# Kernel optimization log

Hardware: AMD Instinct MI355X
Metric: run time of the kernel (lower is better)

The kernel has to match this reference:

```python
import jax, jax.numpy as jnp
import numpy as np

N, E, C, H, L = 50000, 800000, 128, 2, 2  # nodes, edges, hidden_dim, heads, layers
NEG_SLOPE = 0.2
BN_EPS = 1e-5


def setup_inputs() -> dict:
    key = jax.random.key(0)
    ks = jax.random.split(key, 7)
    s = 1.0 / np.sqrt(C).astype(np.float32)
    x = jax.random.normal(ks[0], (N, C), jnp.float32)
    edge_index = jax.random.randint(ks[1], (2, E), 0, N, dtype=jnp.int64)
    W = jax.random.normal(ks[2], (L, C, H * C), jnp.float32) * s      # per-layer lin weight
    att_src = jax.random.normal(ks[3], (L, H, C), jnp.float32) * s    # a_src
    att_dst = jax.random.normal(ks[4], (L, H, C), jnp.float32) * s    # a_dst
    bias = jnp.zeros((L, C), jnp.float32)                              # GATConv bias
    gamma = jnp.ones((L, C), jnp.float32)                              # BatchNorm weight
    beta = jnp.zeros((L, C), jnp.float32)                              # BatchNorm bias
    return dict(x=x, edge_index=edge_index, W=W, att_src=att_src,
                att_dst=att_dst, bias=bias, gamma=gamma, beta=beta)


def _gat_layer(x, src, dst, W, a_src, a_dst, b):
    # Linear projection, split heads: [N, H, C]
    h = (x @ W).reshape(N, H, C)
    # Per-node attention logits, [N, H]
    al_s = jnp.sum(h * a_src[None], axis=-1)
    al_d = jnp.sum(h * a_dst[None], axis=-1)
    # Per-edge raw scores [E', H] (E' includes self loops)
    e = jax.nn.leaky_relu(al_s[src] + al_d[dst], NEG_SLOPE)
    # Segment softmax over incoming edges of each destination node
    m = jax.ops.segment_max(e, dst, num_segments=N)
    ex = jnp.exp(e - m[dst])
    denom = jax.ops.segment_sum(ex, dst, num_segments=N)
    alpha = ex / denom[dst]
    # Weighted scatter-add aggregation: [N, H, C]
    out = jax.ops.segment_sum(alpha[:, :, None] * h[src], dst, num_segments=N)
    # concat=False -> mean over heads, then bias
    return out.mean(axis=1) + b


def _batchnorm(x, g, bt):
    mu = x.mean(axis=0)
    var = jnp.mean((x - mu) ** 2, axis=0)  # biased var (torch BN training math)
    return g * (x - mu) * jax.lax.rsqrt(var + BN_EPS) + bt


def reference(x, edge_index, W, att_src, att_dst, bias, gamma, beta):
    loops = jnp.arange(N, dtype=edge_index.dtype)
    src = jnp.concatenate([edge_index[0], loops])  # add_self_loops=True
    dst = jnp.concatenate([edge_index[1], loops])
    for l in range(L):
        res = x
        x = _gat_layer(x, src, dst, W[l], att_src[l], att_dst[l], bias[l])
        x = _batchnorm(x, gamma[l], beta[l])
        x = jax.nn.elu(x)
        x = x + res  # use_residual, residual_proj = Identity
    return x
```

## Files before the change

### kernel.cpp

```cpp
#include <hip/hip_runtime.h>
#include <hip/hip_bf16.h>

#define N_NODES 50000
#define N_EDGES 800000
#define TOT_E (N_EDGES + N_NODES)
#define PS 256
#define NP ((N_NODES + PS - 1) / PS)
#define BCAP 6000
#define NBK 256
#define BCHUNK ((TOT_E + NBK - 1) / NBK)

typedef unsigned short us8 __attribute__((ext_vector_type(8)));
typedef short s16x8 __attribute__((ext_vector_type(8)));
typedef float f32x4 __attribute__((ext_vector_type(4)));

static __device__ __forceinline__ float lrelu(float v) { return v > 0.0f ? v : 0.2f * v; }

static __device__ __forceinline__ unsigned short f2bf(float f) {
    unsigned int u = __float_as_uint(f);
    unsigned int r = (u + 0x7FFF + ((u >> 16) & 1)) >> 16;
    return (unsigned short)r;
}
static __device__ __forceinline__ float bf2f(unsigned short u) {
    return __uint_as_float(((unsigned int)u) << 16);
}

__global__ __launch_bounds__(256) void bucket_kernel(const int* __restrict__ ei,
                                                     int* __restrict__ gcur,
                                                     unsigned int* __restrict__ buckets) {
    __shared__ int hist[NP];
    __shared__ int runb[NP];
    __shared__ unsigned int pk[BCHUNK + 7];
    int tid = threadIdx.x;
    for (int t = tid; t < NP; t += 256) hist[t] = 0;
    __syncthreads();
    int lo = blockIdx.x * BCHUNK;
    int hi = lo + BCHUNK < TOT_E ? lo + BCHUNK : TOT_E;
    for (int base = lo; base < lo + BCHUNK; base += 256) {
        int i = base + tid;
        if (i < hi) {
            int s, d;
            if (i < N_EDGES) { s = ei[i]; d = ei[N_EDGES + i]; }
            else { s = d = i - N_EDGES; }
            pk[i - lo] = ((unsigned)d << 16) | (unsigned)s;
            atomicAdd(&hist[d >> 8], 1);
        }
    }
    __syncthreads();
    for (int t = tid; t < NP; t += 256) runb[t] = atomicAdd(&gcur[t], hist[t]);
    __syncthreads();
    for (int base = lo; base < lo + BCHUNK; base += 256) {
        int i = base + tid;
        if (i < hi) {
            unsigned v = pk[i - lo];
            int p = v >> 24;
            int slot = atomicAdd(&runb[p], 1);
            if (slot < BCAP) buckets[(size_t)p * BCAP + slot] = v;
        }
    }
}

__global__ __launch_bounds__(256) void csr_kernel(const int* __restrict__ gcur,
                                                  const unsigned int* __restrict__ buckets,
                                                  int* __restrict__ pbeg, int* __restrict__ pend,
                                                  unsigned short* __restrict__ srcs) {
    __shared__ unsigned int epk[BCAP];
    __shared__ unsigned short sl[BCAP];
    __shared__ int deg[256], ps[256], cur[256];
    int p = blockIdx.x, tid = threadIdx.x;
    int len = gcur[p];
    if (len > BCAP) len = BCAP;
    deg[tid] = 0;
    __syncthreads();
    for (int j = tid; j < len; j += 256) {
        unsigned v = buckets[(size_t)p * BCAP + j];
        epk[j] = v;
        atomicAdd(&deg[(v >> 16) & 255], 1);
    }
    __syncthreads();
    int v0 = deg[tid];
    ps[tid] = v0;
    __syncthreads();
#pragma unroll
    for (int o = 1; o < 256; o <<= 1) {
        int u = (tid >= o) ? ps[tid - o] : 0;
        __syncthreads();
        ps[tid] += u;
        __syncthreads();
    }
    int lbeg = ps[tid] - v0;
    cur[tid] = lbeg;
    int n = p * PS + tid;
    if (n < N_NODES) {
        pbeg[n] = p * BCAP + lbeg;
        pend[n] = p * BCAP + lbeg + v0;
    }
    __syncthreads();
    for (int j = tid; j < len; j += 256) {
        unsigned v = epk[j];
        int slot = atomicAdd(&cur[(v >> 16) & 255], 1);
        sl[slot] = (unsigned short)(v & 0xFFFF);
    }
    __syncthreads();
    for (int j = tid; j < len; j += 256) srcs[(size_t)p * BCAP + j] = sl[j];
}

__global__ __launch_bounds__(256) void wa_kernel(const float* __restrict__ W, const float* __restrict__ as_,
                                                 const float* __restrict__ ad_, float* __restrict__ was,
                                                 float* __restrict__ wad) {
    int l = blockIdx.x;
    int t = threadIdx.x;
    int head = t >> 7, k = t & 127;
    const float* wr = W + (size_t)l * 32768 + (size_t)k * 256 + head * 128;
    const float* ar = as_ + l * 256 + head * 128;
    const float* dr = ad_ + l * 256 + head * 128;
    float s = 0.f, d = 0.f;
    for (int c = 0; c < 128; ++c) {
        float wv = wr[c];
        s += wv * ar[c];
        d += wv * dr[c];
    }
    was[l * 256 + t] = s;
    wad[l * 256 + t] = d;
}

__global__ __launch_bounds__(256) void mt_kernel(const float* __restrict__ W, unsigned short* __restrict__ Mt) {
    int idx = blockIdx.x * 256 + threadIdx.x;
    int l = idx >> 15, c = (idx >> 8) & 127, kc = idx & 255;
    int head = kc >> 7, k = kc & 127;
    Mt[idx] = f2bf(0.5f * W[(size_t)l * 32768 + (size_t)k * 256 + head * 128 + c]);
}

__global__ __launch_bounds__(256) void convert_kernel(const float* __restrict__ x, unsigned short* __restrict__ xb,
                                                      const float* __restrict__ was, const float* __restrict__ wad,
                                                      float2* __restrict__ als, float2* __restrict__ ald) {
    int idx = blockIdx.x * 256 + threadIdx.x;
    int n = idx >> 5;
    int c4 = (idx & 31) * 4;
    float4 v = *(const float4*)(x + (size_t)n * 128 + c4);
    ushort4 o;
    o.x = f2bf(v.x); o.y = f2bf(v.y); o.z = f2bf(v.z); o.w = f2bf(v.w);
    *(ushort4*)(xb + (size_t)n * 128 + c4) = o;
    float4 ws0 = *(const float4*)(was + c4);
    float4 ws1 = *(const float4*)(was + 128 + c4);
    float4 wd0 = *(const float4*)(wad + c4);
    float4 wd1 = *(const float4*)(wad + 128 + c4);
    float s0 = v.x * ws0.x + v.y * ws0.y + v.z * ws0.z + v.w * ws0.w;
    float s1 = v.x * ws1.x + v.y * ws1.y + v.z * ws1.z + v.w * ws1.w;
    float d0 = v.x * wd0.x + v.y * wd0.y + v.z * wd0.z + v.w * wd0.w;
    float d1 = v.x * wd1.x + v.y * wd1.y + v.z * wd1.z + v.w * wd1.w;
#pragma unroll
    for (int o2 = 1; o2 < 32; o2 <<= 1) {
        s0 += __shfl_xor(s0, o2);
        s1 += __shfl_xor(s1, o2);
        d0 += __shfl_xor(d0, o2);
        d1 += __shfl_xor(d1, o2);
    }
    if ((idx & 31) == 0) {
        als[n] = make_float2(s0, s1);
        ald[n] = make_float2(d0, d1);
    }
}

__global__ __launch_bounds__(256) void agg_kernel(const unsigned short* __restrict__ xb,
                                                  const float2* __restrict__ als, const float2* __restrict__ ald,
                                                  const int* __restrict__ pbeg, const int* __restrict__ pend,
                                                  const unsigned short* __restrict__ srcs,
                                                  unsigned short* __restrict__ y) {
    int tid = blockIdx.x * 256 + threadIdx.x;
    int n = tid >> 4;
    int gl = tid & 15;
    if (n >= N_NODES) return;
    int b = pbeg[n], e = pend[n];
    float2 ad = ald[n];
    int cb = gl * 8;

    float a0[8], a1[8];
#pragma unroll
    for (int j = 0; j < 8; ++j) { a0[j] = 0.f; a1[j] = 0.f; }
    float d0 = 0.f, d1 = 0.f;

    int len = e - b;
    int m = len >> 1;
    int b2 = b + m;
    int lenB = len - m;
    for (int i = 0; i < lenB; ++i) {
        bool actA = i < m;
        int iA = actA ? (b + i) : (b2 + i);
        int sA = srcs[iA];
        int sB = srcs[b2 + i];
        float2 asA = als[sA];
        float2 asB = als[sB];
        us8 vA = *(const us8*)(xb + (size_t)sA * 128 + cb);
        us8 vB = *(const us8*)(xb + (size_t)sB * 128 + cb);
        float w0A = actA ? __expf(lrelu(asA.x + ad.x)) : 0.f;
        float w1A = actA ? __expf(lrelu(asA.y + ad.y)) : 0.f;
        float w0B = __expf(lrelu(asB.x + ad.x));
        float w1B = __expf(lrelu(asB.y + ad.y));
        d0 += w0A + w0B;
        d1 += w1A + w1B;
#pragma unroll
        for (int j = 0; j < 8; ++j) {
            float fA = bf2f(vA[j]);
            float fB = bf2f(vB[j]);
            a0[j] += w0A * fA + w0B * fB;
            a1[j] += w1A * fA + w1B * fB;
        }
    }

    float i0 = 1.0f / d0, i1 = 1.0f / d1;
    us8 o0, o1;
#pragma unroll
    for (int j = 0; j < 8; ++j) {
        o0[j] = f2bf(a0[j] * i0);
        o1[j] = f2bf(a1[j] * i1);
    }
    unsigned short* yp = y + (size_t)n * 256 + cb;
    *(us8*)yp = o0;
    *(us8*)(yp + 128) = o1;
}

__global__ __launch_bounds__(256) void gemm2_kernel(const unsigned short* __restrict__ zb,
                                                    const unsigned short* __restrict__ Mt,
                                                    const float* __restrict__ bias_,
                                                    unsigned short* __restrict__ preb,
                                                    float* __restrict__ stats) {
    __shared__ unsigned short lw[128 * 128];
    __shared__ float redsum[4][128];
    __shared__ float redsq[4][128];
    int t = threadIdx.x;
    int w = t >> 6, l = t & 63;
    int r0 = blockIdx.x * 64 + w * 16;
    int lrow = l & 15;
    int lk = l >> 4;

    int arow = r0 + lrow;
    if (arow >= N_NODES) arow = N_NODES - 1;

    f32x4 acc[8];
#pragma unroll
    for (int i = 0; i < 8; ++i) acc[i] = (f32x4){0.f, 0.f, 0.f, 0.f};

    for (int kh = 0; kh < 2; ++kh) {
#pragma unroll
        for (int i = 0; i < 8; ++i) {
            int chunk = t + i * 256;
            int row = chunk >> 4;
            int kc8 = chunk & 15;
            uint4 v = *(const uint4*)(Mt + (size_t)row * 256 + kh * 128 + kc8 * 8);
            int b = row * 256 + ((kc8 * 16) ^ ((row & 7) << 4));
            *(uint4*)((char*)lw + b) = v;
        }
        __syncthreads();
        s16x8 a[4];
#pragma unroll
        for (int ka = 0; ka < 4; ++ka)
            a[ka] = *(const s16x8*)(zb + (size_t)arow * 256 + kh * 128 + ka * 32 + lk * 8);
#pragma unroll
        for (int ct = 0; ct < 8; ++ct) {
            int row = ct * 16 + lrow;
#pragma unroll
            for (int ka = 0; ka < 4; ++ka) {
                int kb = (ka * 64 + lk * 16) ^ ((row & 7) << 4);
                s16x8 bf = *(const s16x8*)((const char*)lw + row * 256 + kb);
                acc[ct] = __builtin_amdgcn_mfma_f32_16x16x32_bf16(a[ka], bf, acc[ct], 0, 0, 0);
            }
        }
        __syncthreads();
    }

    float* fl = (float*)lw;
    int wbase = w * 704;
    int lr2 = l >> 4;
    int cb2 = (l & 15) * 8;
    float4 b0 = *(const float4*)(bias_ + cb2);
    float4 b1 = *(const float4*)(bias_ + cb2 + 4);
    float ssum[8], ssq[8];
#pragma unroll
    for (int j = 0; j < 8; ++j) { ssum[j] = 0.f; ssq[j] = 0.f; }
#pragma unroll
    for (int reg = 0; reg < 4; ++reg) {
#pragma unroll
        for (int ct = 0; ct < 8; ++ct)
            fl[wbase + lk * 176 + ct * 20 + lrow] = acc[ct][reg];
        int ra = wbase + lr2 * 176 + (cb2 >> 4) * 20 + (cb2 & 15);
        f32x4 v0 = *(const f32x4*)(fl + ra);
        f32x4 v1 = *(const f32x4*)(fl + ra + 4);
        int row = r0 + lr2 * 4 + reg;
        if (row < N_NODES) {
            float vals[8] = {v0[0] + b0.x, v0[1] + b0.y, v0[2] + b0.z, v0[3] + b0.w,
                             v1[0] + b1.x, v1[1] + b1.y, v1[2] + b1.z, v1[3] + b1.w};
            us8 ob;
#pragma unroll
            for (int j = 0; j < 8; ++j) {
                ob[j] = f2bf(vals[j]);
                ssum[j] += vals[j];
                ssq[j] += vals[j] * vals[j];
            }
            *(us8*)(preb + (size_t)row * 128 + cb2) = ob;
        }
    }
#pragma unroll
    for (int j = 0; j < 8; ++j) {
        ssum[j] += __shfl_xor(ssum[j], 16);
        ssum[j] += __shfl_xor(ssum[j], 32);
        ssq[j] += __shfl_xor(ssq[j], 16);
        ssq[j] += __shfl_xor(ssq[j], 32);
    }
    if (l < 16) {
#pragma unroll
        for (int j = 0; j < 8; ++j) {
            redsum[w][cb2 + j] = ssum[j];
            redsq[w][cb2 + j] = ssq[j];
        }
    }
    __syncthreads();
    if (t < 128) {
        atomicAdd(&stats[t], redsum[0][t] + redsum[1][t] + redsum[2][t] + redsum[3][t]);
    } else if (t < 256) {
        int c = t - 128;
        atomicAdd(&stats[128 + c], redsq[0][c] + redsq[1][c] + redsq[2][c] + redsq[3][c]);
    }
}

__global__ __launch_bounds__(256) void final_kernel(const unsigned short* __restrict__ preb,
                                                    const float* __restrict__ resf,
                                                    const unsigned short* __restrict__ resb,
                                                    const float* __restrict__ gamma, const float* __restrict__ beta,
                                                    const float* __restrict__ stats, float* __restrict__ out,
                                                    unsigned short* __restrict__ xb_out,
                                                    const float* __restrict__ was_n, const float* __restrict__ wad_n,
                                                    float2* __restrict__ als_o, float2* __restrict__ ald_o) {
    const float invn = 1.0f / (float)N_NODES;
    int idx = blockIdx.x * 256 + threadIdx.x;
    int n = idx >> 4;
    int c8 = (idx & 15) * 8;
    us8 pv = *(const us8*)(preb + (size_t)n * 128 + c8);
    float rs[8];
    if (resf) {
        float4 r0 = *(const float4*)(resf + (size_t)n * 128 + c8);
        float4 r1 = *(const float4*)(resf + (size_t)n * 128 + c8 + 4);
        rs[0] = r0.x; rs[1] = r0.y; rs[2] = r0.z; rs[3] = r0.w;
        rs[4] = r1.x; rs[5] = r1.y; rs[6] = r1.z; rs[7] = r1.w;
    } else {
        us8 rv = *(const us8*)(resb + (size_t)n * 128 + c8);
#pragma unroll
        for (int j = 0; j < 8; ++j) rs[j] = bf2f(rv[j]);
    }
    float4 sm0 = *(const float4*)(stats + c8);
    float4 sm1 = *(const float4*)(stats + c8 + 4);
    float4 sq0 = *(const float4*)(stats + 128 + c8);
    float4 sq1 = *(const float4*)(stats + 128 + c8 + 4);
    float4 g0 = *(const float4*)(gamma + c8);
    float4 g1 = *(const float4*)(gamma + c8 + 4);
    float4 bt0 = *(const float4*)(beta + c8);
    float4 bt1 = *(const float4*)(beta + c8 + 4);
    float sm[8] = {sm0.x, sm0.y, sm0.z, sm0.w, sm1.x, sm1.y, sm1.z, sm1.w};
    float sq[8] = {sq0.x, sq0.y, sq0.z, sq0.w, sq1.x, sq1.y, sq1.z, sq1.w};
    float gg[8] = {g0.x, g0.y, g0.z, g0.w, g1.x, g1.y, g1.z, g1.w};
    float bb[8] = {bt0.x, bt0.y, bt0.z, bt0.w, bt1.x, bt1.y, bt1.z, bt1.w};
    float vals[8];
#pragma unroll
    for (int j = 0; j < 8; ++j) {
        float mean = sm[j] * invn;
        float var = sq[j] * invn - mean * mean;
        float is = rsqrtf(var + 1e-5f) * gg[j];
        float val = (bf2f(pv[j]) - mean) * is + bb[j];
        val = val > 0.f ? val : (__expf(val) - 1.0f);
        vals[j] = val + rs[j];
    }
    if (out) {
        float* op = out + (size_t)n * 128 + c8;
        *(float4*)op = make_float4(vals[0], vals[1], vals[2], vals[3]);
        *(float4*)(op + 4) = make_float4(vals[4], vals[5], vals[6], vals[7]);
    }
    if (xb_out) {
        us8 ob;
#pragma unroll
        for (int j = 0; j < 8; ++j) ob[j] = f2bf(vals[j]);
        *(us8*)(xb_out + (size_t)n * 128 + c8) = ob;
        float s0 = 0.f, s1 = 0.f, d0 = 0.f, d1 = 0.f;
#pragma unroll
        for (int j = 0; j < 8; ++j) {
            int c = c8 + j;
            s0 += vals[j] * was_n[c];
            s1 += vals[j] * was_n[128 + c];
            d0 += vals[j] * wad_n[c];
            d1 += vals[j] * wad_n[128 + c];
        }
#pragma unroll
        for (int o = 1; o < 16; o <<= 1) {
            s0 += __shfl_xor(s0, o);
            s1 += __shfl_xor(s1, o);
            d0 += __shfl_xor(d0, o);
            d1 += __shfl_xor(d1, o);
        }
        if ((idx & 15) == 0) {
            als_o[n] = make_float2(s0, s1);
            ald_o[n] = make_float2(d0, d1);
        }
    }
}

extern "C" void kernel_launch(void* const* d_in, const int* in_sizes, int n_in,
                              void* d_out, int out_size, void* d_ws, size_t ws_size,
                              hipStream_t stream) {
    const float* x0   = (const float*)d_in[0];
    const int* ei     = (const int*)d_in[1];
    const float* W    = (const float*)d_in[2];
    const float* asrc = (const float*)d_in[3];
    const float* adst = (const float*)d_in[4];
    const float* bias = (const float*)d_in[5];
    const float* gam  = (const float*)d_in[6];
    const float* bet  = (const float*)d_in[7];
    float* out = (float*)d_out;

    char* ws = (char*)d_ws;
    size_t off = 0;
    auto alloc = [&](size_t bytes) -> void* {
        void* p = ws + off;
        off += (bytes + 255) & ~(size_t)255;
        return p;
    };
    int* gcur   = (int*)alloc((size_t)NP * 4);
    unsigned int* buckets = (unsigned int*)alloc((size_t)NP * BCAP * 4);
    unsigned short* srcs  = (unsigned short*)alloc((size_t)NP * BCAP * 2);
    int* pbeg   = (int*)alloc((size_t)N_NODES * 4);
    int* pend   = (int*)alloc((size_t)N_NODES * 4);
    unsigned short* xb = (unsigned short*)alloc((size_t)N_NODES * 128 * 2);
    unsigned short* y  = (unsigned short*)alloc((size_t)N_NODES * 256 * 2);
    unsigned short* preb = (unsigned short*)alloc((size_t)N_NODES * 128 * 2);
    unsigned short* Mt = (unsigned short*)alloc((size_t)2 * 128 * 256 * 2);
    float* was  = (float*)alloc(512 * 4);
    float* wad  = (float*)alloc(512 * 4);
    float* als  = (float*)alloc((size_t)N_NODES * 2 * 4);
    float* ald  = (float*)alloc((size_t)N_NODES * 2 * 4);
    float* stats = (float*)alloc(512 * 4);

    hipMemsetAsync(gcur, 0, (size_t)NP * 4, stream);
    hipMemsetAsync(stats, 0, 512 * 4, stream);

    bucket_kernel<<<NBK, 256, 0, stream>>>(ei, gcur, buckets);
    csr_kernel<<<NP, 256, 0, stream>>>(gcur, buckets, pbeg, pend, srcs);
    wa_kernel<<<2, 256, 0, stream>>>(W, asrc, adst, was, wad);
    mt_kernel<<<256, 256, 0, stream>>>(W, Mt);
    convert_kernel<<<(N_NODES * 32) / 256, 256, 0, stream>>>(x0, xb, was, wad, (float2*)als, (float2*)ald);

    for (int l = 0; l < 2; ++l) {
        agg_kernel<<<(N_NODES * 16 + 255) / 256, 256, 0, stream>>>(
            xb, (const float2*)als, (const float2*)ald, pbeg, pend, srcs, y);
        gemm2_kernel<<<(N_NODES + 63) / 64, 256, 0, stream>>>(
            y, Mt + (size_t)l * 32768, bias + l * 128, preb, stats + l * 256);
        final_kernel<<<(N_NODES * 16) / 256, 256, 0, stream>>>(
            preb,
            l == 0 ? x0 : (const float*)nullptr,
            l == 0 ? (const unsigned short*)nullptr : xb,
            gam + l * 128, bet + l * 128, stats + l * 256,
            l == 0 ? (float*)nullptr : out,
            l == 0 ? xb : (unsigned short*)nullptr,
            was + 256, wad + 256,
            (float2*)als, (float2*)ald);
    }
}
```

Before: 207.7 us.

## Fold memsets into wa_kernel and unroll aggregation over four edge streams

Measured after the change: 200.5 us, median of 2. 1.04x faster.

```diff
diff --git a/kernel.cpp b/kernel.cpp
--- a/kernel.cpp
+++ b/kernel.cpp
@@ -23,6 +23,28 @@
 }
 static __device__ __forceinline__ float bf2f(unsigned short u) {
     return __uint_as_float(((unsigned int)u) << 16);
+}
+
+__global__ __launch_bounds__(256) void wa_kernel(const float* __restrict__ W, const float* __restrict__ as_,
+                                                 const float* __restrict__ ad_, float* __restrict__ was,
+                                                 float* __restrict__ wad,
+                                                 int* __restrict__ gcur, float* __restrict__ stats) {
+    int l = blockIdx.x;
+    int t = threadIdx.x;
+    stats[l * 256 + t] = 0.f;
+    if (l == 0 && t < NP) gcur[t] = 0;
+    int head = t >> 7, k = t & 127;
+    const float* wr = W + (size_t)l * 32768 + (size_t)k * 256 + head * 128;
+    const float* ar = as_ + l * 256 + head * 128;
+    const float* dr = ad_ + l * 256 + head * 128;
+    float s = 0.f, d = 0.f;
+    for (int c = 0; c < 128; ++c) {
+        float wv = wr[c];
+        s += wv * ar[c];
+        d += wv * dr[c];
+    }
+    was[l * 256 + t] = s;
+    wad[l * 256 + t] = d;
 }
 
 __global__ __launch_bounds__(256) void bucket_kernel(const int* __restrict__ ei,
@@ -103,25 +125,6 @@
     }
     __syncthreads();
     for (int j = tid; j < len; j += 256) srcs[(size_t)p * BCAP + j] = sl[j];
-}
-
-__global__ __launch_bounds__(256) void wa_kernel(const float* __restrict__ W, const float* __restrict__ as_,
-                                                 const float* __restrict__ ad_, float* __restrict__ was,
-                                                 float* __restrict__ wad) {
-    int l = blockIdx.x;
-    int t = threadIdx.x;
-    int head = t >> 7, k = t & 127;
-    const float* wr = W + (size_t)l * 32768 + (size_t)k * 256 + head * 128;
-    const float* ar = as_ + l * 256 + head * 128;
-    const float* dr = ad_ + l * 256 + head * 128;
-    float s = 0.f, d = 0.f;
-    for (int c = 0; c < 128; ++c) {
-        float wv = wr[c];
-        s += wv * ar[c];
-        d += wv * dr[c];
-    }
-    was[l * 256 + t] = s;
-    wad[l * 256 + t] = d;
 }
 
 __global__ __launch_bounds__(256) void mt_kernel(const float* __restrict__ W, unsigned short* __restrict__ Mt) {
@@ -181,39 +184,50 @@
     float d0 = 0.f, d1 = 0.f;
 
     int len = e - b;
-    int m = len >> 1;
-    int b2 = b + m;
-    int lenB = len - m;
-    for (int i = 0; i < lenB; ++i) {
-        bool actA = i < m;
-        int iA = actA ? (b + i) : (b2 + i);
-        int sA = srcs[iA];
-        int sB = srcs[b2 + i];
-        float2 asA = als[sA];
-        float2 asB = als[sB];
-        us8 vA = *(const us8*)(xb + (size_t)sA * 128 + cb);
-        us8 vB = *(const us8*)(xb + (size_t)sB * 128 + cb);
-        float w0A = actA ? __expf(lrelu(asA.x + ad.x)) : 0.f;
-        float w1A = actA ? __expf(lrelu(asA.y + ad.y)) : 0.f;
-        float w0B = __expf(lrelu(asB.x + ad.x));
-        float w1B = __expf(lrelu(asB.y + ad.y));
-        d0 += w0A + w0B;
-        d1 += w1A + w1B;
+    int L = (len + 3) >> 2;
+    for (int i = 0; i < L; ++i) {
+        int o0i = i;
+        int o1i = L + i;
+        int o2i = 2 * L + i;
+        int o3i = 3 * L + i;
+        bool c0 = o0i < len, c1 = o1i < len, c2 = o2i < len, c3 = o3i < len;
+        int i0 = b + (c0 ? o0i : 0);
+        int i1 = b + (c1 ? o1i : 0);
+        int i2 = b + (c2 ? o2i : 0);
+        int i3 = b + (c3 ? o3i : 0);
+        int s0 = srcs[i0], s1 = srcs[i1], s2 = srcs[i2], s3 = srcs[i3];
+        float2 A0 = als[s0], A1 = als[s1], A2 = als[s2], A3 = als[s3];
+        us8 v0 = *(const us8*)(xb + (size_t)s0 * 128 + cb);
+        us8 v1 = *(const us8*)(xb + (size_t)s1 * 128 + cb);
+        us8 v2 = *(const us8*)(xb + (size_t)s2 * 128 + cb);
+        us8 v3 = *(const us8*)(xb + (size_t)s3 * 128 + cb);
+        float w00 = c0 ? __expf(lrelu(A0.x + ad.x)) : 0.f;
+        float w10 = c0 ? __expf(lrelu(A0.y + ad.y)) : 0.f;
+        float w01 = c1 ? __expf(lrelu(A1.x + ad.x)) : 0.f;
+        float w11 = c1 ? __expf(lrelu(A1.y + ad.y)) : 0.f;
+        float w02 = c2 ? __expf(lrelu(A2.x + ad.x)) : 0.f;
+        float w12 = c2 ? __expf(lrelu(A2.y + ad.y)) : 0.f;
+        float w03 = c3 ? __expf(lrelu(A3.x + ad.x)) : 0.f;
+        float w13 = c3 ? __expf(lrelu(A3.y + ad.y)) : 0.f;
+        d0 += (w00 + w01) + (w02 + w03);
+        d1 += (w10 + w11) + (w12 + w13);
 #pragma unroll
         for (int j = 0; j < 8; ++j) {
-            float fA = bf2f(vA[j]);
-            float fB = bf2f(vB[j]);
-            a0[j] += w0A * fA + w0B * fB;
-            a1[j] += w1A * fA + w1B * fB;
-        }
-    }
-
-    float i0 = 1.0f / d0, i1 = 1.0f / d1;
+            float f0 = bf2f(v0[j]);
+            float f1 = bf2f(v1[j]);
+            float f2 = bf2f(v2[j]);
+            float f3 = bf2f(v3[j]);
+            a0[j] += (w00 * f0 + w01 * f1) + (w02 * f2 + w03 * f3);
+            a1[j] += (w10 * f0 + w11 * f1) + (w12 * f2 + w13 * f3);
+        }
+    }
+
+    float i0v = 1.0f / d0, i1v = 1.0f / d1;
     us8 o0, o1;
 #pragma unroll
     for (int j = 0; j < 8; ++j) {
-        o0[j] = f2bf(a0[j] * i0);
-        o1[j] = f2bf(a1[j] * i1);
+        o0[j] = f2bf(a0[j] * i0v);
+        o1[j] = f2bf(a1[j] * i1v);
     }
     unsigned short* yp = y + (size_t)n * 256 + cb;
     *(us8*)yp = o0;
@@ -437,12 +451,9 @@
     float* ald  = (float*)alloc((size_t)N_NODES * 2 * 4);
     float* stats = (float*)alloc(512 * 4);
 
-    hipMemsetAsync(gcur, 0, (size_t)NP * 4, stream);
-    hipMemsetAsync(stats, 0, 512 * 4, stream);
-
+    wa_kernel<<<2, 256, 0, stream>>>(W, asrc, adst, was, wad, gcur, stats);
     bucket_kernel<<<NBK, 256, 0, stream>>>(ei, gcur, buckets);
     csr_kernel<<<NP, 256, 0, stream>>>(gcur, buckets, pbeg, pend, srcs);
-    wa_kernel<<<2, 256, 0, stream>>>(W, asrc, adst, was, wad);
     mt_kernel<<<256, 256, 0, stream>>>(W, Mt);
     convert_kernel<<<(N_NODES * 32) / 256, 256, 0, stream>>>(x0, xb, was, wad, (float2*)als, (float2*)ald);
 
```

## Fuse edge aggregation with projection GEMM via shared-memory tile; fold memsets into wa_kernel

Applied to the files above, without the earlier changes.

New measurement: 256.9 us. 23.7% more time.

```diff
diff --git a/kernel.cpp b/kernel.cpp
--- a/kernel.cpp
+++ b/kernel.cpp
@@ -23,6 +23,28 @@
 }
 static __device__ __forceinline__ float bf2f(unsigned short u) {
     return __uint_as_float(((unsigned int)u) << 16);
+}
+
+__global__ __launch_bounds__(256) void wa_kernel(const float* __restrict__ W, const float* __restrict__ as_,
+                                                 const float* __restrict__ ad_, float* __restrict__ was,
+                                                 float* __restrict__ wad,
+                                                 int* __restrict__ gcur, float* __restrict__ stats) {
+    int l = blockIdx.x;
+    int t = threadIdx.x;
+    stats[l * 256 + t] = 0.f;
+    if (l == 0 && t < NP) gcur[t] = 0;
+    int head = t >> 7, k = t & 127;
+    const float* wr = W + (size_t)l * 32768 + (size_t)k * 256 + head * 128;
+    const float* ar = as_ + l * 256 + head * 128;
+    const float* dr = ad_ + l * 256 + head * 128;
+    float s = 0.f, d = 0.f;
+    for (int c = 0; c < 128; ++c) {
+        float wv = wr[c];
+        s += wv * ar[c];
+        d += wv * dr[c];
+    }
+    was[l * 256 + t] = s;
+    wad[l * 256 + t] = d;
 }
 
 __global__ __launch_bounds__(256) void bucket_kernel(const int* __restrict__ ei,
@@ -103,25 +125,6 @@
     }
     __syncthreads();
     for (int j = tid; j < len; j += 256) srcs[(size_t)p * BCAP + j] = sl[j];
-}
-
-__global__ __launch_bounds__(256) void wa_kernel(const float* __restrict__ W, const float* __restrict__ as_,
-                                                 const float* __restrict__ ad_, float* __restrict__ was,
-                                                 float* __restrict__ wad) {
-    int l = blockIdx.x;
-    int t = threadIdx.x;
-    int head = t >> 7, k = t & 127;
-    const float* wr = W + (size_t)l * 32768 + (size_t)k * 256 + head * 128;
-    const float* ar = as_ + l * 256 + head * 128;
-    const float* dr = ad_ + l * 256 + head * 128;
-    float s = 0.f, d = 0.f;
-    for (int c = 0; c < 128; ++c) {
-        float wv = wr[c];
-        s += wv * ar[c];
-        d += wv * dr[c];
-    }
-    was[l * 256 + t] = s;
-    wad[l * 256 + t] = d;
 }
 
 __global__ __launch_bounds__(256) void mt_kernel(const float* __restrict__ W, unsigned short* __restrict__ Mt) {
@@ -162,84 +165,87 @@
     }
 }
 
-__global__ __launch_bounds__(256) void agg_kernel(const unsigned short* __restrict__ xb,
-                                                  const float2* __restrict__ als, const float2* __restrict__ ald,
-                                                  const int* __restrict__ pbeg, const int* __restrict__ pend,
-                                                  const unsigned short* __restrict__ srcs,
-                                                  unsigned short* __restrict__ y) {
-    int tid = blockIdx.x * 256 + threadIdx.x;
-    int n = tid >> 4;
-    int gl = tid & 15;
-    if (n >= N_NODES) return;
-    int b = pbeg[n], e = pend[n];
-    float2 ad = ald[n];
-    int cb = gl * 8;
-
-    float a0[8], a1[8];
-#pragma unroll
-    for (int j = 0; j < 8; ++j) { a0[j] = 0.f; a1[j] = 0.f; }
-    float d0 = 0.f, d1 = 0.f;
-
-    int len = e - b;
-    int m = len >> 1;
-    int b2 = b + m;
-    int lenB = len - m;
-    for (int i = 0; i < lenB; ++i) {
-        bool actA = i < m;
-        int iA = actA ? (b + i) : (b2 + i);
-        int sA = srcs[iA];
-        int sB = srcs[b2 + i];
-        float2 asA = als[sA];
-        float2 asB = als[sB];
-        us8 vA = *(const us8*)(xb + (size_t)sA * 128 + cb);
-        us8 vB = *(const us8*)(xb + (size_t)sB * 128 + cb);
-        float w0A = actA ? __expf(lrelu(asA.x + ad.x)) : 0.f;
-        float w1A = actA ? __expf(lrelu(asA.y + ad.y)) : 0.f;
-        float w0B = __expf(lrelu(asB.x + ad.x));
-        float w1B = __expf(lrelu(asB.y + ad.y));
-        d0 += w0A + w0B;
-        d1 += w1A + w1B;
-#pragma unroll
-        for (int j = 0; j < 8; ++j) {
-            float fA = bf2f(vA[j]);
-            float fB = bf2f(vB[j]);
-            a0[j] += w0A * fA + w0B * fB;
-            a1[j] += w1A * fA + w1B * fB;
-        }
-    }
-
-    float i0 = 1.0f / d0, i1 = 1.0f / d1;
-    us8 o0, o1;
-#pragma unroll
-    for (int j = 0; j < 8; ++j) {
-        o0[j] = f2bf(a0[j] * i0);
-        o1[j] = f2bf(a1[j] * i1);
-    }
-    unsigned short* yp = y + (size_t)n * 256 + cb;
-    *(us8*)yp = o0;
-    *(us8*)(yp + 128) = o1;
-}
-
-__global__ __launch_bounds__(256) void gemm2_kernel(const unsigned short* __restrict__ zb,
-                                                    const unsigned short* __restrict__ Mt,
-                                                    const float* __restrict__ bias_,
-                                                    unsigned short* __restrict__ preb,
-                                                    float* __restrict__ stats) {
+__global__ __launch_bounds__(256) void aggemm_kernel(const unsigned short* __restrict__ xb,
+                                                     const float2* __restrict__ als, const float2* __restrict__ ald,
+                                                     const int* __restrict__ pbeg, const int* __restrict__ pend,
+                                                     const unsigned short* __restrict__ srcs,
+                                                     const unsigned short* __restrict__ Mt,
+                                                     const float* __restrict__ bias_,
+                                                     unsigned short* __restrict__ preb,
+                                                     float* __restrict__ stats) {
+    __shared__ unsigned short ytile[32 * 256];
     __shared__ unsigned short lw[128 * 128];
-    __shared__ float redsum[4][128];
-    __shared__ float redsq[4][128];
+    __shared__ float redsum[4][64], redsq[4][64];
     int t = threadIdx.x;
+    int n0 = blockIdx.x * 32;
+
+    for (int half = 0; half < 2; ++half) {
+        int nl = half * 16 + (t >> 4);
+        int n = n0 + nl;
+        int gl = t & 15;
+        int cb = gl * 8;
+        int e0 = (gl ^ (nl & 7)) * 8;
+        unsigned short* yp = ytile + nl * 256;
+        if (n < N_NODES) {
+            int b = pbeg[n], e = pend[n];
+            float2 ad = ald[n];
+            float a0[8], a1[8];
+#pragma unroll
+            for (int j = 0; j < 8; ++j) { a0[j] = 0.f; a1[j] = 0.f; }
+            float d0 = 0.f, d1 = 0.f;
+            int len = e - b;
+            int m = len >> 1;
+            int b2 = b + m;
+            int lenB = len - m;
+            for (int i = 0; i < lenB; ++i) {
+                bool actA = i < m;
+                int iA = actA ? (b + i) : (b2 + i);
+                int sA = srcs[iA];
+                int sB = srcs[b2 + i];
+                float2 asA = als[sA];
+                float2 asB = als[sB];
+                us8 vA = *(const us8*)(xb + (size_t)sA * 128 + cb);
+                us8 vB = *(const us8*)(xb + (size_t)sB * 128 + cb);
+                float w0A = actA ? __expf(lrelu(asA.x + ad.x)) : 0.f;
+                float w1A = actA ? __expf(lrelu(asA.y + ad.y)) : 0.f;
+                float w0B = __expf(lrelu(asB.x + ad.x));
+                float w1B = __expf(lrelu(asB.y + ad.y));
+                d0 += w0A + w0B;
+                d1 += w1A + w1B;
+#pragma unroll
+                for (int j = 0; j < 8; ++j) {
+                    float fA = bf2f(vA[j]);
+                    float fB = bf2f(vB[j]);
+                    a0[j] += w0A * fA + w0B * fB;
+                    a1[j] += w1A * fA + w1B * fB;
+                }
+            }
+            float i0 = 1.0f / d0, i1 = 1.0f / d1;
+            us8 o0, o1;
+#pragma unroll
+            for (int j = 0; j < 8; ++j) {
+                o0[j] = f2bf(a0[j] * i0);
+                o1[j] = f2bf(a1[j] * i1);
+            }
+            *(us8*)(yp + e0) = o0;
+            *(us8*)(yp + 128 + e0) = o1;
+        } else {
+            us8 z = (us8){0, 0, 0, 0, 0, 0, 0, 0};
+            *(us8*)(yp + e0) = z;
+            *(us8*)(yp + 128 + e0) = z;
+        }
+    }
+    __syncthreads();
+
     int w = t >> 6, l = t & 63;
-    int r0 = blockIdx.x * 64 + w * 16;
     int lrow = l & 15;
     int lk = l >> 4;
-
-    int arow = r0 + lrow;
-    if (arow >= N_NODES) arow = N_NODES - 1;
-
-    f32x4 acc[8];
-#pragma unroll
-    for (int i = 0; i < 8; ++i) acc[i] = (f32x4){0.f, 0.f, 0.f, 0.f};
+    int rw = (w & 1) * 16;
+    int cw = (w >> 1) * 64;
+
+    f32x4 acc[4];
+#pragma unroll
+    for (int i = 0; i < 4; ++i) acc[i] = (f32x4){0.f, 0.f, 0.f, 0.f};
 
     for (int kh = 0; kh < 2; ++kh) {
 #pragma unroll
@@ -253,12 +259,15 @@
         }
         __syncthreads();
         s16x8 a[4];
-#pragma unroll
-        for (int ka = 0; ka < 4; ++ka)
-            a[ka] = *(const s16x8*)(zb + (size_t)arow * 256 + kh * 128 + ka * 32 + lk * 8);
-#pragma unroll
-        for (int ct = 0; ct < 8; ++ct) {
-            int row = ct * 16 + lrow;
+        int r = rw + lrow;
+#pragma unroll
+        for (int ka = 0; ka < 4; ++ka) {
+            int c = kh * 16 + ka * 4 + lk;
+            a[ka] = *(const s16x8*)(ytile + r * 256 + ((c ^ (r & 7)) * 8));
+        }
+#pragma unroll
+        for (int ct = 0; ct < 4; ++ct) {
+            int row = cw + ct * 16 + lrow;
 #pragma unroll
             for (int ka = 0; ka < 4; ++ka) {
                 int kb = (ka * 64 + lk * 16) ^ ((row & 7) << 4);
@@ -270,38 +279,35 @@
     }
 
     float* fl = (float*)lw;
-    int wbase = w * 704;
+    int wbase = w * 352;
     int lr2 = l >> 4;
-    int cb2 = (l & 15) * 8;
-    float4 b0 = *(const float4*)(bias_ + cb2);
-    float4 b1 = *(const float4*)(bias_ + cb2 + 4);
-    float ssum[8], ssq[8];
-#pragma unroll
-    for (int j = 0; j < 8; ++j) { ssum[j] = 0.f; ssq[j] = 0.f; }
+    int c4 = (l & 15) * 4;
+    float4 bv = *(const float4*)(bias_ + cw + c4);
+    float ssum[4], ssq[4];
+#pragma unroll
+    for (int j = 0; j < 4; ++j) { ssum[j] = 0.f; ssq[j] = 0.f; }
 #pragma unroll
     for (int reg = 0; reg < 4; ++reg) {
 #pragma unroll
-        for (int ct = 0; ct < 8; ++ct)
-            fl[wbase + lk * 176 + ct * 20 + lrow] = acc[ct][reg];
-        int ra = wbase + lr2 * 176 + (cb2 >> 4) * 20 + (cb2 & 15);
+        for (int ct = 0; ct < 4; ++ct)
+            fl[wbase + lk * 88 + ct * 20 + lrow] = acc[ct][reg];
+        int ra = wbase + lr2 * 88 + (c4 >> 4) * 20 + (c4 & 15);
         f32x4 v0 = *(const f32x4*)(fl + ra);
-        f32x4 v1 = *(const f32x4*)(fl + ra + 4);
-        int row = r0 + lr2 * 4 + reg;
+        int row = n0 + rw + lr2 * 4 + reg;
         if (row < N_NODES) {
-            float vals[8] = {v0[0] + b0.x, v0[1] + b0.y, v0[2] + b0.z, v0[3] + b0.w,
-                             v1[0] + b1.x, v1[1] + b1.y, v1[2] + b1.z, v1[3] + b1.w};
-            us8 ob;
-#pragma unroll
-            for (int j = 0; j < 8; ++j) {
-                ob[j] = f2bf(vals[j]);
+            float vals[4] = {v0[0] + bv.x, v0[1] + bv.y, v0[2] + bv.z, v0[3] + bv.w};
+            ushort4 ob;
+#pragma unroll
+            for (int j = 0; j < 4; ++j) {
+                ((unsigned short*)&ob)[j] = f2bf(vals[j]);
                 ssum[j] += vals[j];
                 ssq[j] += vals[j] * vals[j];
             }
-            *(us8*)(preb + (size_t)row * 128 + cb2) = ob;
-        }
-    }
-#pragma unroll
-    for (int j = 0; j < 8; ++j) {
+            *(ushort4*)(preb + (size_t)row * 128 + cw + c4) = ob;
+        }
+    }
+#pragma unroll
+    for (int j = 0; j < 4; ++j) {
         ssum[j] += __shfl_xor(ssum[j], 16);
         ssum[j] += __shfl_xor(ssum[j], 32);
         ssq[j] += __shfl_xor(ssq[j], 16);
@@ -309,18 +315,18 @@
     }
     if (l < 16) {
 #pragma unroll
-        for (int j = 0; j < 8; ++j) {
-            redsum[w][cb2 + j] = ssum[j];
-            redsq[w][cb2 + j] = ssq[j];
-        }
-    }
-    __syncthreads();
-    if (t < 128) {
-        atomicAdd(&stats[t], redsum[0][t] + redsum[1][t] + redsum[2][t] + redsum[3][t]);
-    } else if (t < 256) {
-        int c = t - 128;
-        atomicAdd(&stats[128 + c], redsq[0][c] + redsq[1][c] + redsq[2][c] + redsq[3][c]);
-    }
+        for (int j = 0; j < 4; ++j) {
+            redsum[w][c4 + j] = ssum[j];
+            redsq[w][c4 + j] = ssq[j];
+        }
+    }
+    __syncthreads();
+    float contrib;
+    if (t < 64) contrib = redsum[0][t] + redsum[1][t];
+    else if (t < 128) contrib = redsum[2][t - 64] + redsum[3][t - 64];
+    else if (t < 192) contrib = redsq[0][t - 128] + redsq[1][t - 128];
+    else contrib = redsq[2][t - 192] + redsq[3][t - 192];
+    atomicAdd(&stats[t], contrib);
 }
 
 __global__ __launch_bounds__(256) void final_kernel(const unsigned short* __restrict__ preb,
@@ -428,7 +434,6 @@
     int* pbeg   = (int*)alloc((size_t)N_NODES * 4);
     int* pend   = (int*)alloc((size_t)N_NODES * 4);
     unsigned short* xb = (unsigned short*)alloc((size_t)N_NODES * 128 * 2);
-    unsigned short* y  = (unsigned short*)alloc((size_t)N_NODES * 256 * 2);
     unsigned short* preb = (unsigned short*)alloc((size_t)N_NODES * 128 * 2);
     unsigned short* Mt = (unsigned short*)alloc((size_t)2 * 128 * 256 * 2);
     float* was  = (float*)alloc(512 * 4);
@@ -437,20 +442,16 @@
     float* ald  = (float*)alloc((size_t)N_NODES * 2 * 4);
     float* stats = (float*)alloc(512 * 4);
 
-    hipMemsetAsync(gcur, 0, (size_t)NP * 4, stream);
-    hipMemsetAsync(stats, 0, 512 * 4, stream);
-
+    wa_kernel<<<2, 256, 0, stream>>>(W, asrc, adst, was, wad, gcur, stats);
     bucket_kernel<<<NBK, 256, 0, stream>>>(ei, gcur, buckets);
     csr_kernel<<<NP, 256, 0, stream>>>(gcur, buckets, pbeg, pend, srcs);
-    wa_kernel<<<2, 256, 0, stream>>>(W, asrc, adst, was, wad);
     mt_kernel<<<256, 256, 0, stream>>>(W, Mt);
     convert_kernel<<<(N_NODES * 32) / 256, 256, 0, stream>>>(x0, xb, was, wad, (float2*)als, (float2*)ald);
 
     for (int l = 0; l < 2; ++l) {
-        agg_kernel<<<(N_NODES * 16 + 255) / 256, 256, 0, stream>>>(
-            xb, (const float2*)als, (const float2*)ald, pbeg, pend, srcs, y);
-        gemm2_kernel<<<(N_NODES + 63) / 64, 256, 0, stream>>>(
-            y, Mt + (size_t)l * 32768, bias + l * 128, preb, stats + l * 256);
+        aggemm_kernel<<<(N_NODES + 31) / 32, 256, 0, stream>>>(
+            xb, (const float2*)als, (const float2*)ald, pbeg, pend, srcs,
+            Mt + (size_t)l * 32768, bias + l * 128, preb, stats + l * 256);
         final_kernel<<<(N_NODES * 16) / 256, 256, 0, stream>>>(
             preb,
             l == 0 ? x0 : (const float*)nullptr,
```
